# Kernel tuning notes

Measured on AMD Instinct MI355X. Metric: run time of the kernel, lower is better.

Reference implementation:

```python
import jax, jax.numpy as jnp
import numpy as np

EMB_DIM = 64
B, S, D = 64, 1024, 64

def setup_inputs() -> dict:
    key = jax.random.key(0)
    k1, k2, k3, k4, k5 = jax.random.split(key, 5)
    return {
        "query": jax.random.normal(k1, (B, S, D), dtype=jnp.float32),
        "key": jax.random.normal(k2, (B, S, D), dtype=jnp.float32),
        "value": jax.random.normal(k3, (B, S, D), dtype=jnp.float32),
        "a_key": jax.random.normal(k4, (S, S, D), dtype=jnp.float32),
        "a_value": jax.random.normal(k5, (S, S, D), dtype=jnp.float32),
    }

def reference(query, key, value, a_key, a_value):
    scale = jnp.sqrt(jnp.asarray(EMB_DIM, dtype=query.dtype))
    # standard content-content scores: [B, Sq, Sk]
    qk = jnp.einsum("bqd,bkd->bqk", query, key)
    # relative key scores: a_key is [Sq, Sk, D]; contract over D per query position
    rel_qk = jnp.einsum("bqd,qkd->bqk", query, a_key)
    attn = jax.nn.softmax((qk + rel_qk) / scale, axis=-1)
    # content values + relative values
    qkv = jnp.einsum("bqk,bkd->bqd", attn, value)
    rel_qkv = jnp.einsum("bqk,qkd->bqd", attn, a_value)
    return qkv + rel_qkv, attn
```

## Files before the change

kernel.cpp:

```cpp
#include <hip/hip_runtime.h>
#include <stdint.h>

#define S_ 1024
#define D_ 64
#define B_ 64

typedef short short8 __attribute__((ext_vector_type(8)));
typedef unsigned short ushort8 __attribute__((ext_vector_type(8)));
typedef float f32x4 __attribute__((ext_vector_type(4)));
typedef unsigned short u16;

__device__ __forceinline__ u16 f2bf(float x) {
    uint32_t u = __builtin_bit_cast(uint32_t, x);
    return (u16)((u + 0x7FFFu + ((u >> 16) & 1u)) >> 16);
}
__device__ __forceinline__ float bf2f(u16 b) {
    return __builtin_bit_cast(float, ((uint32_t)b) << 16);
}
__device__ __forceinline__ uint32_t pack2(float a, float b) {
    return (uint32_t)f2bf(a) | ((uint32_t)f2bf(b) << 16);
}
__device__ __forceinline__ int scidx(int row, int k) {
    return (((row << 10) + (k & ~7)) ^ ((row & 15) << 3)) + (k & 7);
}

template <int WS>
__global__ __launch_bounds__(256) void k1_qk(const float* __restrict__ Q,
                                             const float* __restrict__ Kk,
                                             float* __restrict__ qkf,
                                             u16* __restrict__ qkb) {
    __shared__ __align__(16) u16 Qs[128][72];
    __shared__ __align__(16) u16 Ks[128][72];
    const float SCL = 0.18033688011112042f;
    const int bx = blockIdx.x;
    const int b  = bx >> 6;
    const int q0 = ((bx >> 3) & 7) << 7;
    const int k0 = (bx & 7) << 7;
    const int t  = threadIdx.x;
#pragma unroll
    for (int i = 0; i < 8; ++i) {
        int f = (i << 8) + t;
        int row = f >> 4, c = (f & 15) << 2;
        float4 v = *reinterpret_cast<const float4*>(&Q[((size_t)(b * S_ + q0 + row) << 6) + c]);
        *reinterpret_cast<uint2*>(&Qs[row][c]) = make_uint2(pack2(v.x, v.y), pack2(v.z, v.w));
        float4 u = *reinterpret_cast<const float4*>(&Kk[((size_t)(b * S_ + k0 + row) << 6) + c]);
        *reinterpret_cast<uint2*>(&Ks[row][c]) = make_uint2(pack2(u.x, u.y), pack2(u.z, u.w));
    }
    __syncthreads();
    const int l = t & 63, w = t >> 6, lr = l & 15, lg = l >> 4;
    short8 a[2][2];
#pragma unroll
    for (int mi = 0; mi < 2; ++mi)
#pragma unroll
        for (int h = 0; h < 2; ++h)
            a[mi][h] = *reinterpret_cast<const short8*>(&Qs[((w * 2 + mi) << 4) + lr][h * 32 + lg * 8]);
    f32x4 acc[2][8] = {};
#pragma unroll
    for (int n = 0; n < 8; ++n) {
        short8 b0 = *reinterpret_cast<const short8*>(&Ks[(n << 4) + lr][lg * 8]);
        short8 b1 = *reinterpret_cast<const short8*>(&Ks[(n << 4) + lr][32 + lg * 8]);
#pragma unroll
        for (int mi = 0; mi < 2; ++mi) {
            acc[mi][n] = __builtin_amdgcn_mfma_f32_16x16x32_bf16(a[mi][0], b0, acc[mi][n], 0, 0, 0);
            acc[mi][n] = __builtin_amdgcn_mfma_f32_16x16x32_bf16(a[mi][1], b1, acc[mi][n], 0, 0, 0);
        }
    }
#pragma unroll
    for (int mi = 0; mi < 2; ++mi)
#pragma unroll
        for (int n = 0; n < 8; ++n)
#pragma unroll
            for (int r = 0; r < 4; ++r) {
                int qq = q0 + ((w * 2 + mi) << 4) + (lg << 2) + r;
                int kc = k0 + (n << 4) + lr;
                size_t idx = ((size_t)(b * S_ + qq) << 10) + kc;
                if (WS) qkb[idx] = f2bf(acc[mi][n][r] * SCL);
                else    qkf[idx] = acc[mi][n][r] * SCL;
            }
}

__device__ __forceinline__ void tpose_store_p(u16* Tls, int pitch, float4 p,
                                              int kb, int t) {
    const int l = t & 63, lr = l & 15, lg = l >> 4;
    float v0 = p.x, v1 = p.y, v2 = p.z, v3 = p.w;
    float y0 = __shfl_xor(v0, 16), y1 = __shfl_xor(v1, 16),
          y2 = __shfl_xor(v2, 16), y3 = __shfl_xor(v3, 16);
    bool o = (lg & 1);
    float n0 = o ? y1 : v0, n1 = o ? v1 : y0, n2 = o ? y3 : v2, n3 = o ? v3 : y2;
    float z0 = __shfl_xor(n0, 32), z1 = __shfl_xor(n1, 32),
          z2 = __shfl_xor(n2, 32), z3 = __shfl_xor(n3, 32);
    bool h = (lg & 2);
    float T0 = h ? z2 : n0, T1 = h ? z3 : n1, T2 = h ? n2 : z0, T3 = h ? n3 : z1;
    int d = (lr << 2) + lg;
    *reinterpret_cast<uint2*>(&Tls[d * pitch + kb]) = make_uint2(pack2(T0, T1), pack2(T2, T3));
}

template <int WS>
__global__ __launch_bounds__(512) void k2_mid(const float* __restrict__ Q,
                                              const float* __restrict__ AK,
                                              const float* __restrict__ AV,
                                              u16* __restrict__ qkb,
                                              const float* __restrict__ qkf,
                                              float* __restrict__ invg,
                                              float* __restrict__ attn,
                                              float* __restrict__ outp) {
    __shared__ __align__(16) u16 Sc[64 * 1024];
    __shared__ __align__(16) u16 Qs[64][72];
    __shared__ __align__(16) u16 Ak[2][64][72];
    __shared__ float invs[64];
    const float SCL = 0.18033688011112042f;
    const int q = blockIdx.x;
    const int t = threadIdx.x;
    const int l = t & 63, w = t >> 6, lr = l & 15, lg = l >> 4;
    const int wq = w & 3;
    const int wh = w >> 2;
    const int srow = t >> 3, sc8 = (t & 7) << 3;

    {
        const float* qp = &Q[((size_t)(srow * S_ + q) << 6) + sc8];
        float4 a = *reinterpret_cast<const float4*>(qp);
        float4 b = *reinterpret_cast<const float4*>(qp + 4);
        *reinterpret_cast<uint4*>(&Qs[srow][sc8]) =
            make_uint4(pack2(a.x * SCL, a.y * SCL), pack2(a.z * SCL, a.w * SCL),
                       pack2(b.x * SCL, b.y * SCL), pack2(b.z * SCL, b.w * SCL));
    }
    const float* akbase = &AK[(size_t)q << 16];
    float4 pa[2][2];
#define LDK(set, tile) do { const float* p_ = akbase + ((size_t)(tile) << 12) + (srow << 6) + sc8; \
        pa[set][0] = *reinterpret_cast<const float4*>(p_);                                         \
        pa[set][1] = *reinterpret_cast<const float4*>(p_ + 4); } while (0)
#define STAGEK(buf) do {                                                                     \
        *reinterpret_cast<uint4*>(&Ak[buf][srow][sc8]) =                                     \
            make_uint4(pack2(pa[buf][0].x, pa[buf][0].y), pack2(pa[buf][0].z, pa[buf][0].w), \
                       pack2(pa[buf][1].x, pa[buf][1].y), pack2(pa[buf][1].z, pa[buf][1].w)); } while (0)
    LDK(0, 0); LDK(1, 1);
    __syncthreads();
    short8 qa[2][2];
#pragma unroll
    for (int bh = 0; bh < 2; ++bh)
#pragma unroll
        for (int h = 0; h < 2; ++h)
            qa[bh][h] = *reinterpret_cast<const short8*>(
                &Qs[(wh << 5) + (bh << 4) + lr][(h << 5) + (lg << 3)]);
    STAGEK(0);
    __syncthreads();

#pragma unroll 2
    for (int tt = 0; tt < 16; ++tt) {
        const int cur = tt & 1, nxt = cur ^ 1;
        short8 ak0 = *reinterpret_cast<const short8*>(&Ak[cur][(wq << 4) + lr][lg << 3]);
        short8 ak1 = *reinterpret_cast<const short8*>(&Ak[cur][(wq << 4) + lr][32 + (lg << 3)]);
        if (tt < 15) STAGEK(nxt);
        if (tt < 14) LDK(cur, tt + 2);
        int kbase = (tt << 6) + (wq << 4) + (lg << 2);
#pragma unroll
        for (int bh = 0; bh < 2; ++bh) {
            f32x4 c = {};
            c = __builtin_amdgcn_mfma_f32_16x16x32_bf16(ak0, qa[bh][0], c, 0, 0, 0);
            c = __builtin_amdgcn_mfma_f32_16x16x32_bf16(ak1, qa[bh][1], c, 0, 0, 0);
            *reinterpret_cast<uint2*>(&Sc[scidx((wh << 5) + (bh << 4) + lr, kbase)]) =
                make_uint2(pack2(c[0], c[1]), pack2(c[2], c[3]));
        }
        __syncthreads();
    }
#undef LDK
#undef STAGEK

    const float* avbase = &AV[(size_t)q << 16];
    float4 pv[2][2];
#pragma unroll
    for (int s = 0; s < 2; ++s)
#pragma unroll
        for (int i = 0; i < 2; ++i) {
            int f = (i << 9) + t;
            pv[s][i] = *reinterpret_cast<const float4*>(
                &avbase[((size_t)s << 12) + ((size_t)(f >> 4) << 6) + ((f & 15) << 2)]);
        }

    {
        const int ch = t & 7;
        float s = 0.f;
#pragma unroll 4
        for (int i = 0; i < 16; ++i) {
            int k = (((i << 3) + ch) << 3);
            int idx = scidx(srow, k);
            ushort8 rel = *reinterpret_cast<const ushort8*>(&Sc[idx]);
            float g[8];
            if (WS) {
                ushort8 gq = *reinterpret_cast<const ushort8*>(
                    &qkb[((size_t)(srow * S_ + q) << 10) + k]);
#pragma unroll
                for (int jj = 0; jj < 8; ++jj) g[jj] = bf2f(gq[jj]);
            } else {
                const float* qkrow = &qkf[((size_t)(srow * S_ + q) << 10)];
                float4 g0 = *reinterpret_cast<const float4*>(&qkrow[k]);
                float4 g1 = *reinterpret_cast<const float4*>(&qkrow[k + 4]);
                g[0] = g0.x; g[1] = g0.y; g[2] = g0.z; g[3] = g0.w;
                g[4] = g1.x; g[5] = g1.y; g[6] = g1.z; g[7] = g1.w;
            }
            ushort8 e;
#pragma unroll
            for (int jj = 0; jj < 8; ++jj) {
                float ev = exp2f(g[jj] + bf2f(rel[jj]));
                s += ev;
                e[jj] = f2bf(ev);
            }
            *reinterpret_cast<ushort8*>(&Sc[idx]) = e;
            if (WS)
                *reinterpret_cast<ushort8*>(&qkb[((size_t)(srow * S_ + q) << 10) + k]) = e;
        }
        s += __shfl_xor(s, 1); s += __shfl_xor(s, 2); s += __shfl_xor(s, 4);
        if (ch == 0) {
            float inv = 1.0f / s;
            invs[srow] = inv;
            if (WS) invg[srow * S_ + q] = inv;
        }
    }
    __syncthreads();

    tpose_store_p(&Ak[0][0][0], 72, pv[0][0], (w << 2), t);
    tpose_store_p(&Ak[0][0][0], 72, pv[0][1], 32 + (w << 2), t);
    __syncthreads();

    f32x4 oacc[2] = {};
#pragma unroll 2
    for (int tt = 0; tt < 16; ++tt) {
        const int cur = tt & 1, nxt = cur ^ 1;
        short8 bb0 = *reinterpret_cast<const short8*>(&Ak[cur][(wq << 4) + lr][lg << 3]);
        short8 bb1 = *reinterpret_cast<const short8*>(&Ak[cur][(wq << 4) + lr][32 + (lg << 3)]);
        if (tt < 15) {
            tpose_store_p(&Ak[nxt][0][0], 72, pv[nxt][0], (w << 2), t);
            tpose_store_p(&Ak[nxt][0][0], 72, pv[nxt][1], 32 + (w << 2), t);
        }
        if (tt < 14) {
#pragma unroll
            for (int i = 0; i < 2; ++i) {
                int f = (i << 9) + t;
                pv[cur][i] = *reinterpret_cast<const float4*>(
                    &avbase[((size_t)(tt + 2) << 12) + ((size_t)(f >> 4) << 6) + ((f & 15) << 2)]);
            }
        }
        if (!WS) {
            int col = (t & 255) << 2;
#pragma unroll
            for (int rr = 0; rr < 2; ++rr) {
                int row = (tt << 2) + (rr << 1) + (t >> 8);
                uint2 u = *reinterpret_cast<const uint2*>(&Sc[scidx(row, col)]);
                float inv = invs[row];
                float4 o = make_float4(bf2f((u16)(u.x & 0xffff)) * inv,
                                       bf2f((u16)(u.x >> 16)) * inv,
                                       bf2f((u16)(u.y & 0xffff)) * inv,
                                       bf2f((u16)(u.y >> 16)) * inv);
                *reinterpret_cast<float4*>(&attn[((size_t)(row * S_ + q) << 10) + col]) = o;
            }
        }
#pragma unroll
        for (int mi = 0; mi < 2; ++mi) {
            short8 ea0 = *reinterpret_cast<const short8*>(
                &Sc[scidx((wh << 5) + (mi << 4) + lr, (tt << 6) + (lg << 3))]);
            short8 ea1 = *reinterpret_cast<const short8*>(
                &Sc[scidx((wh << 5) + (mi << 4) + lr, (tt << 6) + 32 + (lg << 3))]);
            oacc[mi] = __builtin_amdgcn_mfma_f32_16x16x32_bf16(ea0, bb0, oacc[mi], 0, 0, 0);
            oacc[mi] = __builtin_amdgcn_mfma_f32_16x16x32_bf16(ea1, bb1, oacc[mi], 0, 0, 0);
        }
        __syncthreads();
    }
#pragma unroll
    for (int mi = 0; mi < 2; ++mi)
#pragma unroll
        for (int r = 0; r < 4; ++r) {
            int brow = (wh << 5) + (mi << 4) + (lg << 2) + r;
            outp[((size_t)(brow * S_ + q) << 6) + (wq << 4) + lr] = oacc[mi][r] * invs[brow];
        }
}

template <int WS>
__global__ __launch_bounds__(512) void k3_pv(const float* __restrict__ V,
                                             float* __restrict__ attn,
                                             const u16* __restrict__ P,
                                             const float* __restrict__ invg,
                                             float* __restrict__ outp) {
    __shared__ __align__(16) u16 Vt[64 * 1032];
    __shared__ __align__(16) u16 At[2][64][72];
    const int b  = blockIdx.x >> 2;
    const int qq = blockIdx.x & 3;
    const int t  = threadIdx.x;
    const int l = t & 63, w = t >> 6, lr = l & 15, lg = l >> 4;
    const int wq = w & 3;
    const int dh = w >> 2;
    const int srow = t >> 3, sc8 = (t & 7) << 3;

    for (int kt = 0; kt < 16; ++kt) {
#pragma unroll
        for (int i = 0; i < 2; ++i) {
            int f = (i << 9) + t;
            int row = f >> 4, c = (f & 15) << 2;
            float4 pvv = *reinterpret_cast<const float4*>(
                &V[((size_t)(b * S_ + (kt << 6) + row) << 6) + c]);
            tpose_store_p(&Vt[0], 1032, pvv, (kt << 6) + (i << 5) + (w << 2), t);
        }
    }
    __syncthreads();

    for (int qs = 0; qs < 4; ++qs) {
        const int qsbase = (qq << 8) + (qs << 6);
        f32x4 acc[2] = {};
        if (WS) {
            const u16* prow = &P[((size_t)(b * S_ + qsbase + (wq << 4) + lr) << 10) + (lg << 3)];
            short8 a0b[2], a1b[2];
#define LDPB(buf, kt) do { const u16* p_ = prow + ((kt) << 6);              \
            a0b[buf] = *reinterpret_cast<const short8*>(p_);                \
            a1b[buf] = *reinterpret_cast<const short8*>(p_ + 32); } while (0)
            LDPB(0, 0); LDPB(1, 1);
#pragma unroll 2
            for (int kt = 0; kt < 16; ++kt) {
                const int buf = kt & 1;
                short8 a0 = a0b[buf], a1 = a1b[buf];
                if (kt < 14) LDPB(buf, kt + 2);
                {
                    int col = (t & 255) << 2;
#pragma unroll
                    for (int rr = 0; rr < 2; ++rr) {
                        int row = qsbase + (kt << 2) + (rr << 1) + (t >> 8);
                        uint2 u = *reinterpret_cast<const uint2*>(
                            &P[((size_t)(b * S_ + row) << 10) + col]);
                        float inv = invg[b * S_ + row];
                        float4 o = make_float4(bf2f((u16)(u.x & 0xffff)) * inv,
                                               bf2f((u16)(u.x >> 16)) * inv,
                                               bf2f((u16)(u.y & 0xffff)) * inv,
                                               bf2f((u16)(u.y >> 16)) * inv);
                        *reinterpret_cast<float4*>(&attn[((size_t)(b * S_ + row) << 10) + col]) = o;
                    }
                }
#pragma unroll
                for (int n = 0; n < 2; ++n) {
                    const u16* vb = &Vt[((dh << 5) + (n << 4) + lr) * 1032 + (kt << 6) + (lg << 3)];
                    short8 b0 = *reinterpret_cast<const short8*>(vb);
                    short8 b1 = *reinterpret_cast<const short8*>(vb + 32);
                    acc[n] = __builtin_amdgcn_mfma_f32_16x16x32_bf16(a0, b0, acc[n], 0, 0, 0);
                    acc[n] = __builtin_amdgcn_mfma_f32_16x16x32_bf16(a1, b1, acc[n], 0, 0, 0);
                }
            }
#undef LDPB
            float4 inv4 = *reinterpret_cast<const float4*>(
                &invg[b * S_ + qsbase + (wq << 4) + (lg << 2)]);
            float invr[4] = {inv4.x, inv4.y, inv4.z, inv4.w};
#pragma unroll
            for (int n = 0; n < 2; ++n)
#pragma unroll
                for (int r = 0; r < 4; ++r) {
                    size_t idx = ((size_t)(b * S_ + qsbase + (wq << 4) + (lg << 2) + r) << 6)
                                 + (dh << 5) + (n << 4) + lr;
                    outp[idx] += acc[n][r] * invr[r];
                }
        } else {
            const float* arow = &attn[((size_t)(b * S_ + qsbase + srow) << 10) + sc8];
            float4 pa[2][2];
#define LDA3(set, tile) do { const float* p_ = arow + ((tile) << 6);       \
            pa[set][0] = *reinterpret_cast<const float4*>(p_);             \
            pa[set][1] = *reinterpret_cast<const float4*>(p_ + 4); } while (0)
#define STAGEA(buf) do {                                                                     \
            *reinterpret_cast<uint4*>(&At[buf][srow][sc8]) =                                 \
                make_uint4(pack2(pa[buf][0].x, pa[buf][0].y), pack2(pa[buf][0].z, pa[buf][0].w), \
                           pack2(pa[buf][1].x, pa[buf][1].y), pack2(pa[buf][1].z, pa[buf][1].w)); } while (0)
            LDA3(0, 0); LDA3(1, 1);
            __syncthreads();
            STAGEA(0);
            __syncthreads();
#pragma unroll 2
            for (int kt = 0; kt < 16; ++kt) {
                const int cur = kt & 1, nxt = cur ^ 1;
                short8 a0 = *reinterpret_cast<const short8*>(&At[cur][(wq << 4) + lr][lg << 3]);
                short8 a1 = *reinterpret_cast<const short8*>(&At[cur][(wq << 4) + lr][32 + (lg << 3)]);
                if (kt < 15) STAGEA(nxt);
                if (kt < 14) LDA3(cur, kt + 2);
#pragma unroll
                for (int n = 0; n < 2; ++n) {
                    const u16* vb = &Vt[((dh << 5) + (n << 4) + lr) * 1032 + (kt << 6) + (lg << 3)];
                    short8 b0 = *reinterpret_cast<const short8*>(vb);
                    short8 b1 = *reinterpret_cast<const short8*>(vb + 32);
                    acc[n] = __builtin_amdgcn_mfma_f32_16x16x32_bf16(a0, b0, acc[n], 0, 0, 0);
                    acc[n] = __builtin_amdgcn_mfma_f32_16x16x32_bf16(a1, b1, acc[n], 0, 0, 0);
                }
                __syncthreads();
            }
#undef LDA3
#undef STAGEA
#pragma unroll
            for (int n = 0; n < 2; ++n)
#pragma unroll
                for (int r = 0; r < 4; ++r) {
                    size_t idx = ((size_t)(b * S_ + qsbase + (wq << 4) + (lg << 2) + r) << 6)
                                 + (dh << 5) + (n << 4) + lr;
                    outp[idx] += acc[n][r];
                }
        }
    }
}

extern "C" void kernel_launch(void* const* d_in, const int* in_sizes, int n_in,
                              void* d_out, int out_size, void* d_ws, size_t ws_size,
                              hipStream_t stream) {
    (void)in_sizes; (void)n_in; (void)out_size;
    const float* Q  = (const float*)d_in[0];
    const float* K  = (const float*)d_in[1];
    const float* V  = (const float*)d_in[2];
    const float* AK = (const float*)d_in[3];
    const float* AV = (const float*)d_in[4];
    float* outp = (float*)d_out;
    float* attn = outp + (size_t)B_ * S_ * D_;
    u16*   qkb  = (u16*)d_ws;
    float* invg = (float*)(qkb + (size_t)B_ * S_ * S_);
    const size_t need = (size_t)B_ * S_ * S_ * sizeof(u16)
                      + (size_t)B_ * S_ * sizeof(float);

    if (ws_size >= need) {
        k1_qk<1> <<<dim3(64 * 8 * 8), dim3(256), 0, stream>>>(Q, K, attn, qkb);
        k2_mid<1><<<dim3(1024),       dim3(512), 0, stream>>>(Q, AK, AV, qkb, attn, invg, attn, outp);
        k3_pv<1> <<<dim3(256),        dim3(512), 0, stream>>>(V, attn, qkb, invg, outp);
    } else {
        k1_qk<0> <<<dim3(64 * 8 * 8), dim3(256), 0, stream>>>(Q, K, attn, qkb);
        k2_mid<0><<<dim3(1024),       dim3(512), 0, stream>>>(Q, AK, AV, qkb, attn, invg, attn, outp);
        k3_pv<0> <<<dim3(256),        dim3(512), 0, stream>>>(V, attn, qkb, invg, outp);
    }
}
```

Measured before the change: 373.4 us.

## Halve mid-kernel LDS footprint and move attn write into mid kernel

```diff
diff --git a/kernel.cpp b/kernel.cpp
--- a/kernel.cpp
+++ b/kernel.cpp
@@ -19,6 +19,9 @@
 }
 __device__ __forceinline__ uint32_t pack2(float a, float b) {
     return (uint32_t)f2bf(a) | ((uint32_t)f2bf(b) << 16);
+}
+__device__ __forceinline__ int sidx5(int row, int k) {
+    return (((row << 9) + (k & ~7)) ^ ((row & 15) << 3)) + (k & 7);
 }
 __device__ __forceinline__ int scidx(int row, int k) {
     return (((row << 10) + (k & ~7)) ^ ((row & 15) << 3)) + (k & 7);
@@ -95,13 +98,176 @@
     *reinterpret_cast<uint2*>(&Tls[d * pitch + kb]) = make_uint2(pack2(T0, T1), pack2(T2, T3));
 }
 
-template <int WS>
-__global__ __launch_bounds__(512) void k2_mid(const float* __restrict__ Q,
+__global__ __launch_bounds__(512, 4) void k2_new(const float* __restrict__ Q,
+                                                 const float* __restrict__ AK,
+                                                 const float* __restrict__ AV,
+                                                 u16* __restrict__ qkb,
+                                                 float* __restrict__ invg,
+                                                 float* __restrict__ attn,
+                                                 float* __restrict__ outp) {
+    __shared__ __align__(16) u16 Sc[64 * 512];
+    __shared__ __align__(16) u16 QsAk[64][72];
+    __shared__ float invs[64];
+    const float SCL = 0.18033688011112042f;
+    const int q = blockIdx.x;
+    const int t = threadIdx.x;
+    const int l = t & 63, w = t >> 6, lr = l & 15, lg = l >> 4;
+    const int wq = w & 3;
+    const int wh = w >> 2;
+    const int srow = t >> 3, sc8 = (t & 7) << 3;
+
+    {
+        const float* qp = &Q[((size_t)(srow * S_ + q) << 6) + sc8];
+        float4 a = *reinterpret_cast<const float4*>(qp);
+        float4 b = *reinterpret_cast<const float4*>(qp + 4);
+        *reinterpret_cast<uint4*>(&QsAk[srow][sc8]) =
+            make_uint4(pack2(a.x * SCL, a.y * SCL), pack2(a.z * SCL, a.w * SCL),
+                       pack2(b.x * SCL, b.y * SCL), pack2(b.z * SCL, b.w * SCL));
+    }
+    __syncthreads();
+    short8 qa[2][2];
+#pragma unroll
+    for (int bh = 0; bh < 2; ++bh)
+#pragma unroll
+        for (int h = 0; h < 2; ++h)
+            qa[bh][h] = *reinterpret_cast<const short8*>(
+                &QsAk[(wh << 5) + (bh << 4) + lr][(h << 5) + (lg << 3)]);
+    __syncthreads();
+
+    const float* akbase = &AK[(size_t)q << 16];
+    const float* avbase = &AV[(size_t)q << 16];
+    float4 pa[2];
+    float4 pv[2][2];
+#define LDK(tile) do { const float* p_ = akbase + ((size_t)(tile) << 12) + (srow << 6) + sc8; \
+        pa[0] = *reinterpret_cast<const float4*>(p_);                                         \
+        pa[1] = *reinterpret_cast<const float4*>(p_ + 4); } while (0)
+#define STAGEK() do {                                                                   \
+        *reinterpret_cast<uint4*>(&QsAk[srow][sc8]) =                                   \
+            make_uint4(pack2(pa[0].x, pa[0].y), pack2(pa[0].z, pa[0].w),                \
+                       pack2(pa[1].x, pa[1].y), pack2(pa[1].z, pa[1].w)); } while (0)
+    LDK(0);
+    float ssum = 0.f;
+
+    for (int T = 0; T < 16; ++T) {
+        STAGEK();
+        __syncthreads();
+        if (T < 15) LDK(T + 1);
+        short8 ak0 = *reinterpret_cast<const short8*>(&QsAk[(wq << 4) + lr][lg << 3]);
+        short8 ak1 = *reinterpret_cast<const short8*>(&QsAk[(wq << 4) + lr][32 + (lg << 3)]);
+        int kl = ((T & 7) << 6) + (wq << 4) + (lg << 2);
+#pragma unroll
+        for (int bh = 0; bh < 2; ++bh) {
+            f32x4 c = {};
+            c = __builtin_amdgcn_mfma_f32_16x16x32_bf16(ak0, qa[bh][0], c, 0, 0, 0);
+            c = __builtin_amdgcn_mfma_f32_16x16x32_bf16(ak1, qa[bh][1], c, 0, 0, 0);
+            *reinterpret_cast<uint2*>(&Sc[sidx5((wh << 5) + (bh << 4) + lr, kl)]) =
+                make_uint2(pack2(c[0], c[1]), pack2(c[2], c[3]));
+        }
+        __syncthreads();
+        if (T == 15) {
+#pragma unroll
+            for (int s = 0; s < 2; ++s)
+#pragma unroll
+                for (int i = 0; i < 2; ++i) {
+                    int f = (i << 9) + t;
+                    pv[s][i] = *reinterpret_cast<const float4*>(
+                        &avbase[((size_t)s << 12) + ((size_t)(f >> 4) << 6) + ((f & 15) << 2)]);
+                }
+        }
+        if ((T & 7) == 7) {
+            const int kh = T >> 3;
+            const int ch = t & 7;
+#pragma unroll 4
+            for (int i = 0; i < 8; ++i) {
+                int klc = (((i << 3) + ch) << 3);
+                int kg = (kh << 9) + klc;
+                int idx = sidx5(srow, klc);
+                ushort8 rel = *reinterpret_cast<const ushort8*>(&Sc[idx]);
+                ushort8 gq = *reinterpret_cast<const ushort8*>(
+                    &qkb[((size_t)(srow * S_ + q) << 10) + kg]);
+                ushort8 e;
+#pragma unroll
+                for (int jj = 0; jj < 8; ++jj) {
+                    float ev = exp2f(bf2f(gq[jj]) + bf2f(rel[jj]));
+                    ssum += ev;
+                    e[jj] = f2bf(ev);
+                }
+                *reinterpret_cast<ushort8*>(&qkb[((size_t)(srow * S_ + q) << 10) + kg]) = e;
+            }
+        }
+    }
+#undef LDK
+#undef STAGEK
+    ssum += __shfl_xor(ssum, 1); ssum += __shfl_xor(ssum, 2); ssum += __shfl_xor(ssum, 4);
+    if ((t & 7) == 0) {
+        float inv = 1.0f / ssum;
+        invs[srow] = inv;
+        invg[srow * S_ + q] = inv;
+    }
+    __syncthreads();
+
+    u16* Akb = &Sc[0];
+    tpose_store_p(Akb, 72, pv[0][0], (w << 2), t);
+    tpose_store_p(Akb, 72, pv[0][1], 32 + (w << 2), t);
+    __syncthreads();
+    f32x4 oacc[2] = {};
+#pragma unroll 2
+    for (int tt = 0; tt < 16; ++tt) {
+        const int cur = tt & 1, nxt = cur ^ 1;
+        const u16* Akc = Akb + cur * 4608;
+        short8 bb0 = *reinterpret_cast<const short8*>(&Akc[((wq << 4) + lr) * 72 + (lg << 3)]);
+        short8 bb1 = *reinterpret_cast<const short8*>(&Akc[((wq << 4) + lr) * 72 + 32 + (lg << 3)]);
+        if (tt < 15) {
+            tpose_store_p(Akb + nxt * 4608, 72, pv[nxt][0], (w << 2), t);
+            tpose_store_p(Akb + nxt * 4608, 72, pv[nxt][1], 32 + (w << 2), t);
+        }
+        if (tt < 14) {
+#pragma unroll
+            for (int i = 0; i < 2; ++i) {
+                int f = (i << 9) + t;
+                pv[cur][i] = *reinterpret_cast<const float4*>(
+                    &avbase[((size_t)(tt + 2) << 12) + ((size_t)(f >> 4) << 6) + ((f & 15) << 2)]);
+            }
+        }
+        {
+            int col = (t & 255) << 2;
+#pragma unroll
+            for (int rr = 0; rr < 2; ++rr) {
+                int row = (tt << 2) + (rr << 1) + (t >> 8);
+                uint2 u = *reinterpret_cast<const uint2*>(
+                    &qkb[((size_t)(row * S_ + q) << 10) + col]);
+                float inv = invs[row];
+                float4 o = make_float4(bf2f((u16)(u.x & 0xffff)) * inv,
+                                       bf2f((u16)(u.x >> 16)) * inv,
+                                       bf2f((u16)(u.y & 0xffff)) * inv,
+                                       bf2f((u16)(u.y >> 16)) * inv);
+                *reinterpret_cast<float4*>(&attn[((size_t)(row * S_ + q) << 10) + col]) = o;
+            }
+        }
+#pragma unroll
+        for (int mi = 0; mi < 2; ++mi) {
+            const u16* prow = &qkb[((size_t)(((wh << 5) + (mi << 4) + lr) * S_ + q) << 10)
+                                   + (tt << 6) + (lg << 3)];
+            short8 ea0 = *reinterpret_cast<const short8*>(prow);
+            short8 ea1 = *reinterpret_cast<const short8*>(prow + 32);
+            oacc[mi] = __builtin_amdgcn_mfma_f32_16x16x32_bf16(ea0, bb0, oacc[mi], 0, 0, 0);
+            oacc[mi] = __builtin_amdgcn_mfma_f32_16x16x32_bf16(ea1, bb1, oacc[mi], 0, 0, 0);
+        }
+        __syncthreads();
+    }
+#pragma unroll
+    for (int mi = 0; mi < 2; ++mi)
+#pragma unroll
+        for (int r = 0; r < 4; ++r) {
+            int brow = (wh << 5) + (mi << 4) + (lg << 2) + r;
+            outp[((size_t)(brow * S_ + q) << 6) + (wq << 4) + lr] = oacc[mi][r] * invs[brow];
+        }
+}
+
+__global__ __launch_bounds__(512) void k2_f32(const float* __restrict__ Q,
                                               const float* __restrict__ AK,
                                               const float* __restrict__ AV,
-                                              u16* __restrict__ qkb,
                                               const float* __restrict__ qkf,
-                                              float* __restrict__ invg,
                                               float* __restrict__ attn,
                                               float* __restrict__ outp) {
     __shared__ __align__(16) u16 Sc[64 * 1024];
@@ -112,10 +278,8 @@
     const int q = blockIdx.x;
     const int t = threadIdx.x;
     const int l = t & 63, w = t >> 6, lr = l & 15, lg = l >> 4;
-    const int wq = w & 3;
-    const int wh = w >> 2;
+    const int wq = w & 3, wh = w >> 2;
     const int srow = t >> 3, sc8 = (t & 7) << 3;
-
     {
         const float* qp = &Q[((size_t)(srow * S_ + q) << 6) + sc8];
         float4 a = *reinterpret_cast<const float4*>(qp);
@@ -144,7 +308,6 @@
                 &Qs[(wh << 5) + (bh << 4) + lr][(h << 5) + (lg << 3)]);
     STAGEK(0);
     __syncthreads();
-
 #pragma unroll 2
     for (int tt = 0; tt < 16; ++tt) {
         const int cur = tt & 1, nxt = cur ^ 1;
@@ -165,7 +328,6 @@
     }
 #undef LDK
 #undef STAGEK
-
     const float* avbase = &AV[(size_t)q << 16];
     float4 pv[2][2];
 #pragma unroll
@@ -176,7 +338,6 @@
             pv[s][i] = *reinterpret_cast<const float4*>(
                 &avbase[((size_t)s << 12) + ((size_t)(f >> 4) << 6) + ((f & 15) << 2)]);
         }
-
     {
         const int ch = t & 7;
         float s = 0.f;
@@ -185,19 +346,10 @@
             int k = (((i << 3) + ch) << 3);
             int idx = scidx(srow, k);
             ushort8 rel = *reinterpret_cast<const ushort8*>(&Sc[idx]);
-            float g[8];
-            if (WS) {
-                ushort8 gq = *reinterpret_cast<const ushort8*>(
-                    &qkb[((size_t)(srow * S_ + q) << 10) + k]);
-#pragma unroll
-                for (int jj = 0; jj < 8; ++jj) g[jj] = bf2f(gq[jj]);
-            } else {
-                const float* qkrow = &qkf[((size_t)(srow * S_ + q) << 10)];
-                float4 g0 = *reinterpret_cast<const float4*>(&qkrow[k]);
-                float4 g1 = *reinterpret_cast<const float4*>(&qkrow[k + 4]);
-                g[0] = g0.x; g[1] = g0.y; g[2] = g0.z; g[3] = g0.w;
-                g[4] = g1.x; g[5] = g1.y; g[6] = g1.z; g[7] = g1.w;
-            }
+            const float* qkrow = &qkf[((size_t)(srow * S_ + q) << 10)];
+            float4 g0 = *reinterpret_cast<const float4*>(&qkrow[k]);
+            float4 g1 = *reinterpret_cast<const float4*>(&qkrow[k + 4]);
+            float g[8] = {g0.x, g0.y, g0.z, g0.w, g1.x, g1.y, g1.z, g1.w};
             ushort8 e;
 #pragma unroll
             for (int jj = 0; jj < 8; ++jj) {
@@ -206,22 +358,14 @@
                 e[jj] = f2bf(ev);
             }
             *reinterpret_cast<ushort8*>(&Sc[idx]) = e;
-            if (WS)
-                *reinterpret_cast<ushort8*>(&qkb[((size_t)(srow * S_ + q) << 10) + k]) = e;
         }
         s += __shfl_xor(s, 1); s += __shfl_xor(s, 2); s += __shfl_xor(s, 4);
-        if (ch == 0) {
-            float inv = 1.0f / s;
-            invs[srow] = inv;
-            if (WS) invg[srow * S_ + q] = inv;
-        }
-    }
-    __syncthreads();
-
+        if (ch == 0) invs[srow] = 1.0f / s;
+    }
+    __syncthreads();
     tpose_store_p(&Ak[0][0][0], 72, pv[0][0], (w << 2), t);
     tpose_store_p(&Ak[0][0][0], 72, pv[0][1], 32 + (w << 2), t);
     __syncthreads();
-
     f32x4 oacc[2] = {};
 #pragma unroll 2
     for (int tt = 0; tt < 16; ++tt) {
@@ -240,7 +384,7 @@
                     &avbase[((size_t)(tt + 2) << 12) + ((size_t)(f >> 4) << 6) + ((f & 15) << 2)]);
             }
         }
-        if (!WS) {
+        {
             int col = (t & 255) << 2;
 #pragma unroll
             for (int rr = 0; rr < 2; ++rr) {
@@ -276,7 +420,7 @@
 
 template <int WS>
 __global__ __launch_bounds__(512) void k3_pv(const float* __restrict__ V,
-                                             float* __restrict__ attn,
+                                             const float* __restrict__ attn,
                                              const u16* __restrict__ P,
                                              const float* __restrict__ invg,
                                              float* __restrict__ outp) {
@@ -317,21 +461,6 @@
                 const int buf = kt & 1;
                 short8 a0 = a0b[buf], a1 = a1b[buf];
                 if (kt < 14) LDPB(buf, kt + 2);
-                {
-                    int col = (t & 255) << 2;
-#pragma unroll
-                    for (int rr = 0; rr < 2; ++rr) {
-                        int row = qsbase + (kt << 2) + (rr << 1) + (t >> 8);
-                        uint2 u = *reinterpret_cast<const uint2*>(
-                            &P[((size_t)(b * S_ + row) << 10) + col]);
-                        float inv = invg[b * S_ + row];
-                        float4 o = make_float4(bf2f((u16)(u.x & 0xffff)) * inv,
-                                               bf2f((u16)(u.x >> 16)) * inv,
-                                               bf2f((u16)(u.y & 0xffff)) * inv,
-                                               bf2f((u16)(u.y >> 16)) * inv);
-                        *reinterpret_cast<float4*>(&attn[((size_t)(b * S_ + row) << 10) + col]) = o;
-                    }
-                }
 #pragma unroll
                 for (int n = 0; n < 2; ++n) {
                     const u16* vb = &Vt[((dh << 5) + (n << 4) + lr) * 1032 + (kt << 6) + (lg << 3)];
@@ -415,12 +544,12 @@
                       + (size_t)B_ * S_ * sizeof(float);
 
     if (ws_size >= need) {
-        k1_qk<1> <<<dim3(64 * 8 * 8), dim3(256), 0, stream>>>(Q, K, attn, qkb);
-        k2_mid<1><<<dim3(1024),       dim3(512), 0, stream>>>(Q, AK, AV, qkb, attn, invg, attn, outp);
-        k3_pv<1> <<<dim3(256),        dim3(512), 0, stream>>>(V, attn, qkb, invg, outp);
+        k1_qk<1><<<dim3(64 * 8 * 8), dim3(256), 0, stream>>>(Q, K, attn, qkb);
+        k2_new  <<<dim3(1024),       dim3(512), 0, stream>>>(Q, AK, AV, qkb, invg, attn, outp);
+        k3_pv<1><<<dim3(256),        dim3(512), 0, stream>>>(V, attn, qkb, invg, outp);
     } else {
-        k1_qk<0> <<<dim3(64 * 8 * 8), dim3(256), 0, stream>>>(Q, K, attn, qkb);
-        k2_mid<0><<<dim3(1024),       dim3(512), 0, stream>>>(Q, AK, AV, qkb, attn, invg, attn, outp);
-        k3_pv<0> <<<dim3(256),        dim3(512), 0, stream>>>(V, attn, qkb, invg, outp);
-    }
-}
+        k1_qk<0><<<dim3(64 * 8 * 8), dim3(256), 0, stream>>>(Q, K, attn, qkb);
+        k2_f32  <<<dim3(1024),       dim3(512), 0, stream>>>(Q, AK, AV, attn, attn, outp);
+        k3_pv<0><<<dim3(256),        dim3(512), 0, stream>>>(V, attn, qkb, invg, outp);
+    }
+}
```

Measured after the change: 389.2 us. 4.3% more time.
